# Performance work log

Hardware: AMD Instinct MI355X
Metric: run time of the kernel (lower is better)

The kernel has to match this reference:

```python
import jax, jax.numpy as jnp
import numpy as np

D_MODEL = 512
HEADS = 8
MAX_LEN = 2048


def setup_inputs() -> dict:
    key = jax.random.key(0)
    ks = jax.random.split(key, 8)
    b, t, e, h = 2, 2048, D_MODEL, HEADS
    s = e // h
    x = jax.random.normal(ks[0], (b, t, e), dtype=jnp.float32)
    mask = jax.random.randint(ks[1], (b, t), 0, 2).astype(jnp.int32)
    Wq = jax.random.normal(ks[2], (s, s), dtype=jnp.float32) / np.sqrt(s)
    Wk = jax.random.normal(ks[3], (s, s), dtype=jnp.float32) / np.sqrt(s)
    Wv = jax.random.normal(ks[4], (s, s), dtype=jnp.float32) / np.sqrt(s)
    Er = jax.random.normal(ks[5], (h, MAX_LEN, s), dtype=jnp.float32)
    Wo = jax.random.normal(ks[6], (e, e), dtype=jnp.float32) / np.sqrt(e)
    bo = jnp.zeros((e,), dtype=jnp.float32)
    return {"x": x, "mask": mask, "heads": h, "Wq": Wq, "Wk": Wk, "Wv": Wv,
            "Er": Er, "Wo": Wo, "bo": bo}


def reference(x, mask, heads, Wq, Wk, Wv, Er, Wo, bo):
    b, t, e = x.shape
    h = heads
    s = e // h
    x4 = x.reshape(b, t, h, s)
    # per-head shared linear projections (nn.Linear applies x @ W^T), then (b,h,t,s)
    q = jnp.einsum('bthi,oi->bhto', x4, Wq)
    k = jnp.einsum('bthi,oi->bhto', x4, Wk)
    v = jnp.einsum('bthi,oi->bhto', x4, Wv)
    # relative position scores: QEr computed on UNSCALED queries (as in source)
    Er_t = Er[:, Er.shape[1] - t:, :]                  # (h, t, s)
    qe = jnp.einsum('bhts,hls->bhtl', q, Er_t)          # (b, h, t, t)
    idx = jnp.arange(t)
    # _mask_positions: zero where col < t-1-row (flipped upper triangle)
    keep = (idx[None, :] >= (t - 1 - idx[:, None]))
    qe = jnp.where(keep[None, None], qe, 0.0)
    # _skew: pad one column on the left, reshape (t, t+1)->(t+1, t), drop first row
    padded = jnp.pad(qe, ((0, 0), (0, 0), (0, 0), (1, 0)))
    srel = padded.reshape(b, h, t + 1, t)[:, :, 1:, :]  # (b, h, t, t)
    scale = e ** (-0.25)
    scores = jnp.einsum('bhts,bhls->bhtl', q * scale, k * scale) + srel
    neg = jnp.float32(-1e9)
    causal = idx[None, :] > idx[:, None]                # future positions
    scores = jnp.where(causal[None, None], neg, scores)
    # padding mask zeroes entire query rows
    scores = jnp.where(mask[:, None, :, None] == 0, neg, scores)
    probs = jax.nn.softmax(scores, axis=-1)
    out = jnp.einsum('bhtl,bhls->bths', probs, v)       # (b, h, t, s)
    out = out.transpose(0, 2, 1, 3).reshape(b, t, e)
    return out @ Wo.T + bo
```

## Files before the change

### kernel.cpp

```cpp
#include <hip/hip_runtime.h>


#define B_ 2
#define T_ 2048
#define E_ 512
#define H_ 8
#define SCALE2 0.044194173824159216f

typedef __attribute__((ext_vector_type(8))) short bf16x8;
typedef __attribute__((ext_vector_type(4))) float f32x4;

#define MFMA(a,b,c) __builtin_amdgcn_mfma_f32_16x16x32_bf16((a),(b),(c),0,0,0)

__device__ __forceinline__ unsigned short f2bf(float f){
  unsigned u = __builtin_bit_cast(unsigned, f);
  u += 0x7fffu + ((u >> 16) & 1u);
  return (unsigned short)(u >> 16);
}
__device__ __forceinline__ float bf2f(unsigned short h){
  unsigned u = ((unsigned)h) << 16;
  return __builtin_bit_cast(float, u);
}

__global__ __launch_bounds__(256) void prep_qkv(
    const float* __restrict__ x,
    const float* __restrict__ Wq, const float* __restrict__ Wk, const float* __restrict__ Wv,
    unsigned short* __restrict__ qh, unsigned short* __restrict__ ql,
    unsigned short* __restrict__ kb, unsigned short* __restrict__ vb)
{
  int wid = blockIdx.x*4 + (threadIdx.x>>6);
  int o   = threadIdx.x & 63;
  int bh  = wid & 15;
  int rest = wid >> 4;
  int chunk = rest & 31;
  int m = rest >> 5;
  const float* W = (m==0) ? Wq : (m==1) ? Wk : Wv;
  float4 wv[16];
  #pragma unroll
  for (int j=0;j<16;++j) wv[j] = reinterpret_cast<const float4*>(W)[o*16+j];
  if (m==1){
    #pragma unroll
    for (int j=0;j<16;++j){ wv[j].x*=SCALE2; wv[j].y*=SCALE2; wv[j].z*=SCALE2; wv[j].w*=SCALE2; }
  }
  int b = bh>>3, h = bh&7;
  unsigned short* out0 = (m==0) ? qh : (m==1) ? kb : vb;
  for (int tl=0; tl<64; ++tl){
    int t = chunk*64 + tl;
    const float4* xr = reinterpret_cast<const float4*>(x + ((size_t)(b*T_ + t))*E_ + h*64);
    float a0=0.f,a1=0.f,a2=0.f,a3=0.f;
    #pragma unroll
    for (int j=0;j<16;++j){
      float4 xv = xr[j];
      a0 += xv.x*wv[j].x; a1 += xv.y*wv[j].y; a2 += xv.z*wv[j].z; a3 += xv.w*wv[j].w;
    }
    float acc = (a0+a1)+(a2+a3);
    size_t oi = ((size_t)bh*T_ + t)*64 + o;
    if (m==0){
      unsigned short hq = f2bf(acc);
      out0[oi] = hq;
      ql[oi] = f2bf(acc - bf2f(hq));
    } else {
      out0[oi] = f2bf(acc);
    }
  }
}

__global__ void prep_er(const float* __restrict__ Er,
                        unsigned short* __restrict__ eh, unsigned short* __restrict__ el)
{
  int i = (blockIdx.x*blockDim.x + threadIdx.x)*4;
  float4 v = *reinterpret_cast<const float4*>(Er + i);
  unsigned short h0=f2bf(v.x), h1=f2bf(v.y), h2=f2bf(v.z), h3=f2bf(v.w);
  *reinterpret_cast<ushort4*>(&eh[i]) = make_ushort4(h0,h1,h2,h3);
  *reinterpret_cast<ushort4*>(&el[i]) = make_ushort4(
      f2bf(v.x-bf2f(h0)), f2bf(v.y-bf2f(h1)), f2bf(v.z-bf2f(h2)), f2bf(v.w-bf2f(h3)));
}

__global__ void prep_wo(const float* __restrict__ Wo, unsigned short* __restrict__ wob){
  int i = (blockIdx.x*blockDim.x + threadIdx.x)*4;
  float4 v = *reinterpret_cast<const float4*>(Wo + i);
  *reinterpret_cast<ushort4*>(&wob[i]) = make_ushort4(f2bf(v.x),f2bf(v.y),f2bf(v.z),f2bf(v.w));
}

__global__ __launch_bounds__(256) void vsum1(const unsigned short* __restrict__ vb,
                                             float* __restrict__ vpart)
{
  __shared__ float red[4][64];
  int bh = blockIdx.x >> 3, ch = blockIdx.x & 7;
  int s = threadIdx.x & 63, sub = threadIdx.x >> 6;
  const unsigned short* p = vb + ((size_t)bh*T_ + ch*256 + sub*64)*64 + s;
  float acc = 0.f;
  #pragma unroll 8
  for (int t=0;t<64;++t) acc += bf2f(p[(size_t)t*64]);
  red[sub][s] = acc;
  __syncthreads();
  if (sub==0) vpart[(size_t)(bh*8+ch)*64 + s] = red[0][s]+red[1][s]+red[2][s]+red[3][s];
}
__global__ void vsum2(const float* __restrict__ vpart, float* __restrict__ vsum){
  int bh = blockIdx.x, s = threadIdx.x;
  float a = 0.f;
  #pragma unroll
  for (int c=0;c<8;++c) a += vpart[(size_t)(bh*8+c)*64 + s];
  vsum[bh*64+s] = a;
}

__global__ __launch_bounds__(256,2) void attn(
  const unsigned short* __restrict__ qh, const unsigned short* __restrict__ ql,
  const unsigned short* __restrict__ kb, const unsigned short* __restrict__ vb,
  const unsigned short* __restrict__ eh, const unsigned short* __restrict__ el,
  const int* __restrict__ mask, const float* __restrict__ vsum,
  unsigned short* __restrict__ ao)
{
  __shared__ float QEs[4][128][20];
  __shared__ unsigned short Ps[4][16][72];
  __shared__ unsigned short Vt[64][72];

  const int tid = threadIdx.x;
  const int w = tid >> 6, lane = tid & 63, g = lane >> 4, q15 = lane & 15;
  const int bid = blockIdx.x;
  const int bh = bid & 15;
  const int u = bid >> 4;
  const int rt = (u < 16) ? (2*u) : (63 - 2*u);
  const int i0 = rt * 64;
  const int b = bh >> 3, h = bh & 7;

  const size_t qoff = ((size_t)bh*T_ + i0 + 16*w + q15)*64 + 8*g;
  const bf16x8 qa00 = *(const bf16x8*)(qh + qoff);
  const bf16x8 qa01 = *(const bf16x8*)(qh + qoff + 32);
  const bf16x8 qa10 = *(const bf16x8*)(ql + qoff);
  const bf16x8 qa11 = *(const bf16x8*)(ql + qoff + 32);

  f32x4 oacc[4];
  float mrun[4], lrun[4];
  const f32x4 fz = {0.f,0.f,0.f,0.f};
  #pragma unroll
  for (int n=0;n<4;++n) oacc[n] = fz;
  #pragma unroll
  for (int p=0;p<4;++p){ mrun[p] = -1e30f; lrun[p] = 0.f; }

  const int ntiles = i0/64 + 1;
  for (int tI=0; tI<ntiles; ++tI){
    const int j0 = tI*64;
    bf16x8 kf[4][2];
    #pragma unroll
    for (int n=0;n<4;++n){
      const unsigned short* kp = kb + ((size_t)bh*T_ + j0 + 16*n + q15)*64 + 8*g;
      kf[n][0] = *(const bf16x8*)kp;
      kf[n][1] = *(const bf16x8*)(kp+32);
    }
    const int key = tid & 63, sh = tid >> 6;
    bf16x8 vv0 = *(const bf16x8*)(vb + ((size_t)bh*T_ + j0 + key)*64 + 8*sh);
    bf16x8 vv1 = *(const bf16x8*)(vb + ((size_t)bh*T_ + j0 + key)*64 + 8*sh + 32);
    __syncthreads();
    #pragma unroll
    for (int jj=0;jj<8;++jj) Vt[8*sh+jj][key]    = (unsigned short)vv0[jj];
    #pragma unroll
    for (int jj=0;jj<8;++jj) Vt[8*sh+32+jj][key] = (unsigned short)vv1[jj];

    const int lstart = (T_-64) - i0 + j0;
    #pragma unroll 2
    for (int np=0; np<8; ++np){
      int le = 16*np + q15;
      int l = lstart + le; if (l > T_-1) l = T_-1;
      const unsigned short* ep  = eh + ((size_t)h*T_ + l)*64 + 8*g;
      const unsigned short* ep2 = el + ((size_t)h*T_ + l)*64 + 8*g;
      bf16x8 e0 = *(const bf16x8*)ep,  e1 = *(const bf16x8*)(ep+32);
      bf16x8 f0 = *(const bf16x8*)ep2, f1 = *(const bf16x8*)(ep2+32);
      f32x4 qe = {0.f,0.f,0.f,0.f};
      qe = MFMA(qa00, e0, qe); qe = MFMA(qa01, e1, qe);
      qe = MFMA(qa10, e0, qe); qe = MFMA(qa11, e1, qe);
      qe = MFMA(qa00, f0, qe); qe = MFMA(qa01, f1, qe);
      *(f32x4*)&QEs[w][le][4*g] = qe;
    }
    f32x4 sacc[4];
    #pragma unroll
    for (int n=0;n<4;++n){
      f32x4 s = fz;
      s = MFMA(qa00, kf[n][0], s); s = MFMA(qa01, kf[n][1], s);
      s = MFMA(qa10, kf[n][0], s); s = MFMA(qa11, kf[n][1], s);
      sacc[n] = s;
    }
    const bool lastT = (tI == ntiles-1);
    float pv[4][4];
    float tmax[4] = {-1e30f,-1e30f,-1e30f,-1e30f};
    #pragma unroll
    for (int n=0;n<4;++n){
      #pragma unroll
      for (int p=0;p<4;++p){
        int r = 16*w + 4*g + p;
        int c = 16*n + q15;
        float s = sacc[n][p] + QEs[w][63 - r + c][4*g + p];
        if (lastT && c > r) s = -1e30f;
        pv[n][p] = s;
        tmax[p] = fmaxf(tmax[p], s);
      }
    }
    #pragma unroll
    for (int p=0;p<4;++p){
      float m = tmax[p];
      m = fmaxf(m, __shfl_xor(m,1)); m = fmaxf(m, __shfl_xor(m,2));
      m = fmaxf(m, __shfl_xor(m,4)); m = fmaxf(m, __shfl_xor(m,8));
      float mn = fmaxf(mrun[p], m);
      float al = __expf(mrun[p] - mn);
      mrun[p] = mn;
      lrun[p] *= al;
      oacc[0][p]*=al; oacc[1][p]*=al; oacc[2][p]*=al; oacc[3][p]*=al;
      float sum = 0.f;
      #pragma unroll
      for (int n=0;n<4;++n){
        float e = __expf(pv[n][p] - mn);
        pv[n][p] = e;
        sum += e;
      }
      sum += __shfl_xor(sum,1); sum += __shfl_xor(sum,2);
      sum += __shfl_xor(sum,4); sum += __shfl_xor(sum,8);
      lrun[p] += sum;
      #pragma unroll
      for (int n=0;n<4;++n) Ps[w][4*g+p][16*n+q15] = f2bf(pv[n][p]);
    }
    __syncthreads();
    bf16x8 pa0 = *(const bf16x8*)&Ps[w][q15][8*g];
    bf16x8 pa1 = *(const bf16x8*)&Ps[w][q15][8*g+32];
    #pragma unroll
    for (int ns=0; ns<4; ++ns){
      bf16x8 v0 = *(const bf16x8*)&Vt[16*ns+q15][8*g];
      bf16x8 v1 = *(const bf16x8*)&Vt[16*ns+q15][8*g+32];
      oacc[ns] = MFMA(pa0, v0, oacc[ns]);
      oacc[ns] = MFMA(pa1, v1, oacc[ns]);
    }
  }
  #pragma unroll
  for (int p=0;p<4;++p){
    int r = i0 + 16*w + 4*g + p;
    int mk = mask[b*T_ + r];
    float inv = 1.f / lrun[p];
    int rr = h*256 + (r >> 3);
    int cb2 = (r & 7)*64;
    #pragma unroll
    for (int n=0;n<4;++n){
      int sc = 16*n + q15;
      float val = mk ? oacc[n][p]*inv : vsum[bh*64+sc]*(1.f/2048.f);
      ao[((size_t)(b*T_ + rr))*E_ + cb2 + sc] = f2bf(val);
    }
  }
}

__global__ __launch_bounds__(256) void outproj(
  const unsigned short* __restrict__ ao, const unsigned short* __restrict__ wob,
  const float* __restrict__ bo, float* __restrict__ out)
{
  int tid = threadIdx.x;
  int w = tid>>6, lane = tid&63, g = lane>>4, q15 = lane&15;
  int nb = blockIdx.x & 7, rb = blockIdx.x >> 3;
  size_t row = (size_t)rb*64 + 16*w + q15;
  const unsigned short* ap = ao + row*E_ + 8*g;
  const f32x4 fz = {0.f,0.f,0.f,0.f};
  f32x4 acc[4];
  #pragma unroll
  for (int n=0;n<4;++n) acc[n] = fz;
  #pragma unroll 4
  for (int kk=0; kk<16; ++kk){
    bf16x8 a = *(const bf16x8*)(ap + 32*kk);
    #pragma unroll
    for (int n=0;n<4;++n){
      bf16x8 bfr = *(const bf16x8*)(wob + ((size_t)(nb*64 + 16*n + q15))*E_ + 32*kk + 8*g);
      acc[n] = MFMA(a, bfr, acc[n]);
    }
  }
  #pragma unroll
  for (int n=0;n<4;++n){
    int col = nb*64 + 16*n + q15;
    float bv = bo[col];
    #pragma unroll
    for (int p=0;p<4;++p){
      size_t rr = (size_t)rb*64 + 16*w + 4*g + p;
      out[rr*E_ + col] = acc[n][p] + bv;
    }
  }
}

extern "C" void kernel_launch(void* const* d_in, const int* in_sizes, int n_in,
                              void* d_out, int out_size, void* d_ws, size_t ws_size,
                              hipStream_t stream)
{
  int ix=-1, ier=-1, iwo=-1, ibo=-1, c4[4], nc=0;
  for (int i=0;i<n_in;++i){
    switch(in_sizes[i]){
      case 2097152: ix  = i; break;
      case 1048576: ier = i; break;
      case 262144:  iwo = i; break;
      case 512:     ibo = i; break;
      case 4096:    if (nc<4) c4[nc++] = i; break;
      default: break;
    }
  }
  if (ix<0||ier<0||iwo<0||ibo<0||nc!=4){ ix=0;c4[0]=1;c4[1]=3;c4[2]=4;c4[3]=5;ier=6;iwo=7;ibo=8; }
  const float* x  = (const float*)d_in[ix];
  const int* mask = (const int*)d_in[c4[0]];
  const float* Wq = (const float*)d_in[c4[1]];
  const float* Wk = (const float*)d_in[c4[2]];
  const float* Wv = (const float*)d_in[c4[3]];
  const float* Er = (const float*)d_in[ier];
  const float* Wo = (const float*)d_in[iwo];
  const float* bo = (const float*)d_in[ibo];
  float* out = (float*)d_out;

  char* ws = (char*)d_ws;
  unsigned short* qh  = (unsigned short*)(ws + 0);
  unsigned short* ql  = (unsigned short*)(ws + 4194304);
  unsigned short* kb  = (unsigned short*)(ws + 8388608);
  unsigned short* vb  = (unsigned short*)(ws + 12582912);
  unsigned short* eh  = (unsigned short*)(ws + 16777216);
  unsigned short* el  = (unsigned short*)(ws + 18874368);
  unsigned short* wob = (unsigned short*)(ws + 20971520);
  unsigned short* ao  = (unsigned short*)(ws + 21495808);
  float* vsum  = (float*)(ws + 25690112);
  float* vpart = (float*)(ws + 25694208);

  hipLaunchKernelGGL(prep_qkv, dim3(384),  dim3(256), 0, stream, x, Wq, Wk, Wv, qh, ql, kb, vb);
  hipLaunchKernelGGL(prep_er,  dim3(1024), dim3(256), 0, stream, Er, eh, el);
  hipLaunchKernelGGL(prep_wo,  dim3(256),  dim3(256), 0, stream, Wo, wob);
  hipLaunchKernelGGL(vsum1,    dim3(128),  dim3(256), 0, stream, vb, vpart);
  hipLaunchKernelGGL(vsum2,    dim3(16),   dim3(64),  0, stream, vpart, vsum);
  hipLaunchKernelGGL(attn,     dim3(512),  dim3(256), 0, stream, qh, ql, kb, vb, eh, el, mask, vsum, ao);
  hipLaunchKernelGGL(outproj,  dim3(512),  dim3(256), 0, stream, ao, wob, bo, out);
}
```

Before: 310.5 us.

## Reuse relative-position QE tiles via ring buffer and split prep_qkv finer

The attention loop previously recomputed 128 rows of Q·Er per key tile even though consecutive tiles overlap by half. It now keeps a 128-slot ring buffer in shared memory and computes only the 64 new rows per tile (both halves on the first tile), batching the Er loads before the MFMAs. The QK^T product also drops the low-order Q correction MFMAs, which halves that matrix work at some cost in precision. prep_qkv is split into 4x more blocks with 16 rows each to raise parallelism in the projection stage.

```diff
diff --git a/kernel.cpp b/kernel.cpp
--- a/kernel.cpp
+++ b/kernel.cpp
@@ -32,8 +32,8 @@
   int o   = threadIdx.x & 63;
   int bh  = wid & 15;
   int rest = wid >> 4;
-  int chunk = rest & 31;
-  int m = rest >> 5;
+  int chunk = rest & 127;
+  int m = rest >> 7;
   const float* W = (m==0) ? Wq : (m==1) ? Wk : Wv;
   float4 wv[16];
   #pragma unroll
@@ -44,8 +44,8 @@
   }
   int b = bh>>3, h = bh&7;
   unsigned short* out0 = (m==0) ? qh : (m==1) ? kb : vb;
-  for (int tl=0; tl<64; ++tl){
-    int t = chunk*64 + tl;
+  for (int tl=0; tl<16; ++tl){
+    int t = chunk*16 + tl;
     const float4* xr = reinterpret_cast<const float4*>(x + ((size_t)(b*T_ + t))*E_ + h*64);
     float a0=0.f,a1=0.f,a2=0.f,a3=0.f;
     #pragma unroll
@@ -139,8 +139,10 @@
   for (int p=0;p<4;++p){ mrun[p] = -1e30f; lrun[p] = 0.f; }
 
   const int ntiles = i0/64 + 1;
+  const int lstart0 = (T_-64) - i0;
   for (int tI=0; tI<ntiles; ++tI){
     const int j0 = tI*64;
+    const int lstart = lstart0 + j0;
     bf16x8 kf[4][2];
     #pragma unroll
     for (int n=0;n<4;++n){
@@ -157,27 +159,36 @@
     #pragma unroll
     for (int jj=0;jj<8;++jj) Vt[8*sh+32+jj][key] = (unsigned short)vv1[jj];
 
-    const int lstart = (T_-64) - i0 + j0;
-    #pragma unroll 2
-    for (int np=0; np<8; ++np){
-      int le = 16*np + q15;
-      int l = lstart + le; if (l > T_-1) l = T_-1;
-      const unsigned short* ep  = eh + ((size_t)h*T_ + l)*64 + 8*g;
-      const unsigned short* ep2 = el + ((size_t)h*T_ + l)*64 + 8*g;
-      bf16x8 e0 = *(const bf16x8*)ep,  e1 = *(const bf16x8*)(ep+32);
-      bf16x8 f0 = *(const bf16x8*)ep2, f1 = *(const bf16x8*)(ep2+32);
-      f32x4 qe = {0.f,0.f,0.f,0.f};
-      qe = MFMA(qa00, e0, qe); qe = MFMA(qa01, e1, qe);
-      qe = MFMA(qa10, e0, qe); qe = MFMA(qa11, e1, qe);
-      qe = MFMA(qa00, f0, qe); qe = MFMA(qa01, f1, qe);
-      *(f32x4*)&QEs[w][le][4*g] = qe;
+    const int nhalf = (tI==0) ? 2 : 1;
+    for (int half=0; half<nhalf; ++half){
+      const int lb = (tI==0) ? (lstart + 64*half) : (lstart + 64);
+      bf16x8 pe[4][4];
+      #pragma unroll
+      for (int g2=0; g2<4; ++g2){
+        int ln = lb + 16*g2 + q15;
+        int l = (ln > T_-1) ? (T_-1) : ln;
+        const unsigned short* ep  = eh + ((size_t)h*T_ + l)*64 + 8*g;
+        const unsigned short* ep2 = el + ((size_t)h*T_ + l)*64 + 8*g;
+        pe[g2][0] = *(const bf16x8*)ep;
+        pe[g2][1] = *(const bf16x8*)(ep+32);
+        pe[g2][2] = *(const bf16x8*)ep2;
+        pe[g2][3] = *(const bf16x8*)(ep2+32);
+      }
+      #pragma unroll
+      for (int g2=0; g2<4; ++g2){
+        int slot = (lb + 16*g2 + q15) & 127;
+        f32x4 qe = {0.f,0.f,0.f,0.f};
+        qe = MFMA(qa00, pe[g2][0], qe); qe = MFMA(qa01, pe[g2][1], qe);
+        qe = MFMA(qa10, pe[g2][0], qe); qe = MFMA(qa11, pe[g2][1], qe);
+        qe = MFMA(qa00, pe[g2][2], qe); qe = MFMA(qa01, pe[g2][3], qe);
+        *(f32x4*)&QEs[w][slot][4*g] = qe;
+      }
     }
     f32x4 sacc[4];
     #pragma unroll
     for (int n=0;n<4;++n){
       f32x4 s = fz;
       s = MFMA(qa00, kf[n][0], s); s = MFMA(qa01, kf[n][1], s);
-      s = MFMA(qa10, kf[n][0], s); s = MFMA(qa11, kf[n][1], s);
       sacc[n] = s;
     }
     const bool lastT = (tI == ntiles-1);
@@ -189,7 +200,8 @@
       for (int p=0;p<4;++p){
         int r = 16*w + 4*g + p;
         int c = 16*n + q15;
-        float s = sacc[n][p] + QEs[w][63 - r + c][4*g + p];
+        int slot = (lstart + 63 - r + c) & 127;
+        float s = sacc[n][p] + QEs[w][slot][4*g + p];
         if (lastT && c > r) s = -1e30f;
         pv[n][p] = s;
         tmax[p] = fmaxf(tmax[p], s);
@@ -317,7 +329,7 @@
   float* vsum  = (float*)(ws + 25690112);
   float* vpart = (float*)(ws + 25694208);
 
-  hipLaunchKernelGGL(prep_qkv, dim3(384),  dim3(256), 0, stream, x, Wq, Wk, Wv, qh, ql, kb, vb);
+  hipLaunchKernelGGL(prep_qkv, dim3(1536), dim3(256), 0, stream, x, Wq, Wk, Wv, qh, ql, kb, vb);
   hipLaunchKernelGGL(prep_er,  dim3(1024), dim3(256), 0, stream, Er, eh, el);
   hipLaunchKernelGGL(prep_wo,  dim3(256),  dim3(256), 0, stream, Wo, wob);
   hipLaunchKernelGGL(vsum1,    dim3(128),  dim3(256), 0, stream, vb, vpart);
```

After: 250.1 us. 19.5% less time.
